# Kernel tuning notes

Measured on AMD Instinct MI355X. Metric: run time of the kernel, lower is better.

## Reference

```python
import jax, jax.numpy as jnp
import numpy as np

N_NODES = 100000
N_EDGES = 1600000
NEG_SLOPE = 0.2
EPS = 1e-16


def gat_conv(x, edge_index, W, att_src, att_dst, bias, heads, out_ch, concat):
    # x: [N, F_in]; edge_index: [2, E] with edge (src j -> dst i)
    N = x.shape[0]
    src, dst = edge_index[0], edge_index[1]
    h = (x @ W).reshape(N, heads, out_ch)              # [N, H, C]
    a_src = (h * att_src[None]).sum(-1)                # [N, H]
    a_dst = (h * att_dst[None]).sum(-1)                # [N, H]
    e = a_src[src] + a_dst[dst]                        # [E, H]
    e = jnp.where(e > 0, e, NEG_SLOPE * e)             # LeakyReLU(0.2)
    # segment softmax over destination node
    m = jax.ops.segment_max(e, dst, num_segments=N)    # [N, H]
    m = jnp.where(jnp.isfinite(m), m, 0.0)
    ex = jnp.exp(e - m[dst])                           # [E, H]
    s = jax.ops.segment_sum(ex, dst, num_segments=N)   # [N, H]
    alpha = ex / (s[dst] + EPS)                        # [E, H]
    msg = h[src] * alpha[..., None]                    # [E, H, C]
    out = jax.ops.segment_sum(msg, dst, num_segments=N)  # [N, H, C]
    if concat:
        out = out.reshape(N, heads * out_ch)
    else:
        out = out.mean(axis=1)
    return out + bias


def setup_inputs() -> dict:
    key = jax.random.key(0)
    ks = jax.random.split(key, 8)
    x = jax.random.normal(ks[0], (N_NODES, 2), dtype=jnp.float32)
    edge_index = jax.random.randint(ks[1], (2, N_EDGES), 0, N_NODES, dtype=jnp.int64)
    glorot = lambda k, shape, fan: jax.random.normal(k, shape, jnp.float32) * (1.0 / np.sqrt(fan))
    W1 = glorot(ks[2], (2, 128), 2)
    att_src1 = glorot(ks[3], (8, 16), 16)
    att_dst1 = glorot(ks[4], (8, 16), 16)
    b1 = jnp.zeros((128,), jnp.float32)
    W2 = glorot(ks[5], (128, 4), 128)
    att_src2 = glorot(ks[6], (1, 4), 4)
    att_dst2 = glorot(ks[7], (1, 4), 4)
    b2 = jnp.zeros((4,), jnp.float32)
    return {"x": x, "edge_index": edge_index, "W1": W1, "att_src1": att_src1,
            "att_dst1": att_dst1, "b1": b1, "W2": W2, "att_src2": att_src2,
            "att_dst2": att_dst2, "b2": b2}


def reference(x, edge_index, W1, att_src1, att_dst1, b1, W2, att_src2, att_dst2, b2):
    h = gat_conv(x, edge_index, W1, att_src1, att_dst1, b1, heads=8, out_ch=16, concat=True)
    h = jax.nn.relu(h)
    # dropout p=0.6 is identity in eval mode
    h = gat_conv(h, edge_index, W2, att_src2, att_dst2, b2, heads=1, out_ch=4, concat=True)
    return jax.nn.log_softmax(h, axis=1)
```

## Files before the change

### kernel.cpp

```cpp
#include <hip/hip_runtime.h>
#include <math.h>

static constexpr float kNegSlope = 0.2f;
static constexpr float kEps = 1e-16f;
static constexpr int SLICES = 256;
static constexpr int BSHIFT = 7;
static constexpr int BMASK = 127;
static constexpr unsigned SRCMASK = 0x1FFFFu;
static constexpr int CAP = 2816;

__device__ __forceinline__ float leaky(float v) {
    return v > 0.0f ? v : kNegSlope * v;
}


__global__ __launch_bounds__(512) void k_hist1(const int* __restrict__ ei,
                                               int* __restrict__ table,
                                               int* __restrict__ rowptr,
                                               int E, int N, int NBUCK) {
    __shared__ int hist[832];
    int b = blockIdx.x, t = threadIdx.x;
    if (b == 0 && t == 0) rowptr[N] = E;
    for (int i = t; i < NBUCK; i += 512) hist[i] = 0;
    __syncthreads();
    int S = (((E + SLICES - 1) / SLICES) + 3) & ~3;
    int lo = b * S, hi = min(lo + S, E);
    for (int i = lo + t * 4; i < hi; i += 512 * 4) {
        int4 dv = *(const int4*)(ei + E + i);
        atomicAdd(&hist[dv.x >> BSHIFT], 1);
        atomicAdd(&hist[dv.y >> BSHIFT], 1);
        atomicAdd(&hist[dv.z >> BSHIFT], 1);
        atomicAdd(&hist[dv.w >> BSHIFT], 1);
    }
    __syncthreads();
    for (int i = t; i < NBUCK; i += 512) table[i * SLICES + b] = hist[i];
}

__global__ __launch_bounds__(256) void k_scan_reduce(const int* __restrict__ src,
                                                     int* __restrict__ partial, int n) {
    __shared__ int wsum[4];
    int b = blockIdx.x, t = threadIdx.x;
    int base = b * 1024 + t * 4;
    int s = 0;
#pragma unroll
    for (int k = 0; k < 4; ++k) {
        int idx = base + k;
        s += (idx < n) ? src[idx] : 0;
    }
#pragma unroll
    for (int off = 1; off < 64; off <<= 1) s += __shfl_xor(s, off);
    if ((t & 63) == 0) wsum[t >> 6] = s;
    __syncthreads();
    if (t == 0) partial[b] = wsum[0] + wsum[1] + wsum[2] + wsum[3];
}

__global__ __launch_bounds__(256) void k_scan_apply(int* __restrict__ data,
                                                    const int* __restrict__ partial,
                                                    int n, int nsb) {
    __shared__ int sm[8];
    __shared__ int baseSh;
    int b = blockIdx.x, t = threadIdx.x;
    int acc = 0;
    for (int i = t; i < b; i += 256) acc += partial[i];
#pragma unroll
    for (int off = 1; off < 64; off <<= 1) acc += __shfl_xor(acc, off);
    if ((t & 63) == 0) sm[t >> 6] = acc;
    __syncthreads();
    if (t == 0) baseSh = sm[0] + sm[1] + sm[2] + sm[3];
    __syncthreads();
    int chunkBase = baseSh;
    __syncthreads();
    int base = b * 1024 + t * 4;
    int v[4];
#pragma unroll
    for (int k = 0; k < 4; ++k) {
        int idx = base + k;
        v[k] = (idx < n) ? data[idx] : 0;
    }
    int sum4 = v[0] + v[1] + v[2] + v[3];
    int s = sum4;
#pragma unroll
    for (int off = 1; off < 64; off <<= 1) {
        int u = __shfl_up(s, off);
        if ((t & 63) >= off) s += u;
    }
    if ((t & 63) == 63) sm[t >> 6] = s;
    __syncthreads();
    int woff = 0;
    int w = t >> 6;
    for (int ww = 0; ww < w; ++ww) woff += sm[ww];
    int ex = chunkBase + woff + (s - sum4);
#pragma unroll
    for (int k = 0; k < 4; ++k) {
        int idx = base + k;
        if (idx < n) data[idx] = ex;
        ex += v[k];
    }
}

__global__ __launch_bounds__(512) void k_bin2(const int* __restrict__ ei,
                                              const int* __restrict__ table,
                                              unsigned* __restrict__ sbuf, int E, int NBUCK) {
    __shared__ int cur[832];
    int b = blockIdx.x, t = threadIdx.x;
    for (int i = t; i < NBUCK; i += 512) cur[i] = table[i * SLICES + b];
    __syncthreads();
    int S = (((E + SLICES - 1) / SLICES) + 3) & ~3;
    int lo = b * S, hi = min(lo + S, E);
    for (int i = lo + t * 4; i < hi; i += 512 * 4) {
        int4 sv = *(const int4*)(ei + i);
        int4 dv = *(const int4*)(ei + E + i);
        int pos;
        pos = atomicAdd(&cur[dv.x >> BSHIFT], 1);
        sbuf[pos] = (unsigned)sv.x | ((unsigned)(dv.x & BMASK) << 17);
        pos = atomicAdd(&cur[dv.y >> BSHIFT], 1);
        sbuf[pos] = (unsigned)sv.y | ((unsigned)(dv.y & BMASK) << 17);
        pos = atomicAdd(&cur[dv.z >> BSHIFT], 1);
        sbuf[pos] = (unsigned)sv.z | ((unsigned)(dv.z & BMASK) << 17);
        pos = atomicAdd(&cur[dv.w >> BSHIFT], 1);
        sbuf[pos] = (unsigned)sv.w | ((unsigned)(dv.w & BMASK) << 17);
    }
}

__global__ __launch_bounds__(512) void k_sort(
        const unsigned* __restrict__ sbuf, const int* __restrict__ table,
        int* __restrict__ rowptr, int* __restrict__ ssrc,
        int N, int E, int NBUCK) {
    __shared__ int hist[128];
    __shared__ int sc[128];
    __shared__ int cur[128];
    __shared__ unsigned raws[CAP];
    __shared__ int sls[CAP];
    int b = blockIdx.x;
    int t = threadIdx.x;
    int lo = table[b * SLICES];
    int hi = (b + 1 < NBUCK) ? table[(b + 1) * SLICES] : E;
    int cnt = hi - lo;
    bool inLds = (cnt <= CAP);

    if (t < 128) hist[t] = 0;
    __syncthreads();

    if (inLds) {
        for (int i = t; i < cnt; i += 512) {
            unsigned v = sbuf[lo + i];
            raws[i] = v;
            atomicAdd(&hist[v >> 17], 1);
        }
    } else {
        for (int i = lo + t; i < hi; i += 512) atomicAdd(&hist[sbuf[i] >> 17], 1);
    }
    __syncthreads();

    if (t < 128) {
        int lane = t & 63;
        int own = hist[t];
        int v = own;
#pragma unroll
        for (int off = 1; off < 64; off <<= 1) {
            int u = __shfl_up(v, off);
            if (lane >= off) v += u;
        }
        sc[t] = v;
    }
    __syncthreads();
    if (t < 128) {
        int ex = sc[t] - hist[t] + (t >= 64 ? sc[63] : 0);
        cur[t] = ex;
        int node = (b << BSHIFT) + t;
        if (node < N) rowptr[node] = lo + ex;
    }
    __syncthreads();

    if (inLds) {
        for (int i = t; i < cnt; i += 512) {
            unsigned v = raws[i];
            int pos = atomicAdd(&cur[v >> 17], 1);
            sls[pos] = (int)(v & SRCMASK);
        }
        __syncthreads();
        for (int i = t; i < cnt; i += 512) ssrc[lo + i] = sls[i];
    } else {
        for (int i = lo + t; i < hi; i += 512) {
            unsigned v = sbuf[i];
            int pos = atomicAdd(&cur[v >> 17], 1);
            ssrc[lo + pos] = (int)(v & SRCMASK);
        }
    }
}

__global__ __launch_bounds__(256) void k_fill(const int* __restrict__ ssrc,
                                              const float* __restrict__ x,
                                              float* __restrict__ sxy, int E) {
    int i4 = (blockIdx.x * 256 + threadIdx.x) * 4;
    const float2* x2 = (const float2*)x;
    if (i4 + 3 < E) {
        int4 s = *(const int4*)(ssrc + i4);
        float2 a = x2[s.x];
        float2 b = x2[s.y];
        float2 c = x2[s.z];
        float2 d = x2[s.w];
        *(float4*)(sxy + 2 * i4)     = make_float4(a.x, a.y, b.x, b.y);
        *(float4*)(sxy + 2 * i4 + 4) = make_float4(c.x, c.y, d.x, d.y);
    } else {
        for (int i = i4; i < E; ++i) {
            float2 a = x2[ssrc[i]];
            sxy[2 * i] = a.x;
            sxy[2 * i + 1] = a.y;
        }
    }
}

__global__ __launch_bounds__(256) void k_gather1(
        const int* __restrict__ rowptr, const float* __restrict__ sxy,
        const float* __restrict__ x,
        const float* __restrict__ W1, const float* __restrict__ att_src1,
        const float* __restrict__ att_dst1, const float* __restrict__ b1,
        const float* __restrict__ W2, float* __restrict__ h2, int N) {
    __shared__ float pbuf[32];
    int t = threadIdx.x;
    if (t < 32) {
        int which = t >> 4;
        int hd = t & 15;
        int h = hd >> 1, d = hd & 1;
        const float* att = which ? att_dst1 : att_src1;
        float s = 0.0f;
#pragma unroll
        for (int c = 0; c < 16; ++c) s += W1[d * 128 + h * 16 + c] * att[h * 16 + c];
        pbuf[which * 16 + d * 8 + h] = s;
    }
    __syncthreads();

    int idx = blockIdx.x * blockDim.x + t;
    int n = idx >> 3, q = idx & 7;
    if (n >= N) return;
    const float2* x2 = (const float2*)x;
    const float2* sx2 = (const float2*)sxy;
    int start = rowptr[n], end = rowptr[n + 1];
    float2 xn = x2[n];
    float Ps0[8], Ps1[8], adv[8], l[8], s0[8], s1[8];
#pragma unroll
    for (int h = 0; h < 8; ++h) {
        Ps0[h] = pbuf[h];
        Ps1[h] = pbuf[8 + h];
        adv[h] = xn.x * pbuf[16 + h] + xn.y * pbuf[24 + h];
        l[h] = 0.f; s0[h] = 0.f; s1[h] = 0.f;
    }
    for (int j = start + q; j < end; j += 8) {
        float2 xs = sx2[j];
#pragma unroll
        for (int h = 0; h < 8; ++h) {
            float p = __expf(leaky(xs.x * Ps0[h] + xs.y * Ps1[h] + adv[h]));
            l[h] += p; s0[h] += p * xs.x; s1[h] += p * xs.y;
        }
    }
#pragma unroll
    for (int off = 1; off < 8; off <<= 1) {
#pragma unroll
        for (int h = 0; h < 8; ++h) {
            l[h] += __shfl_xor(l[h], off);
            s0[h] += __shfl_xor(s0[h], off);
            s1[h] += __shfl_xor(s1[h], off);
        }
    }
    float h0 = 0.f, h1v = 0.f, h2v = 0.f, h3 = 0.f;
    {
        float inv = 1.0f / (l[q] + kEps);
        float sX0 = s0[q] * inv, sX1 = s1[q] * inv;
#pragma unroll
        for (int c = 0; c < 16; ++c) {
            int col = q * 16 + c;
            float o = fmaxf(W1[col] * sX0 + W1[128 + col] * sX1 + b1[col], 0.0f);
            h0 += o * W2[col * 4 + 0];
            h1v += o * W2[col * 4 + 1];
            h2v += o * W2[col * 4 + 2];
            h3 += o * W2[col * 4 + 3];
        }
    }
#pragma unroll
    for (int off = 1; off < 8; off <<= 1) {
        h0 += __shfl_xor(h0, off);
        h1v += __shfl_xor(h1v, off);
        h2v += __shfl_xor(h2v, off);
        h3 += __shfl_xor(h3, off);
    }
    if (q == 0) {
        ((float4*)h2)[n] = make_float4(h0, h1v, h2v, h3);
    }
}

__global__ __launch_bounds__(256) void k_gather2_out(
        const int* __restrict__ rowptr, const int* __restrict__ ssrc,
        const float* __restrict__ h2, const float* __restrict__ att_src2,
        const float* __restrict__ att_dst2, const float* __restrict__ b2,
        float* __restrict__ out, int N) {
    int idx = blockIdx.x * blockDim.x + threadIdx.x;
    int n = idx >> 3, q = idx & 7;
    if (n >= N) return;
    int start = rowptr[n], end = rowptr[n + 1];
    float4 as2 = *(const float4*)att_src2;
    float4 ad2v = *(const float4*)att_dst2;
    const float4* h4 = (const float4*)h2;
    float4 hn = h4[n];
    float ad = hn.x * ad2v.x + hn.y * ad2v.y + hn.z * ad2v.z + hn.w * ad2v.w;
    float l = 0.0f;
    float4 acc = make_float4(0.f, 0.f, 0.f, 0.f);
    int j = start + q;
    for (; j + 8 < end; j += 16) {
        int s0 = ssrc[j];
        int s1 = ssrc[j + 8];
        float4 ha = h4[s0];
        float4 hb = h4[s1];
        float e0 = ha.x * as2.x + ha.y * as2.y + ha.z * as2.z + ha.w * as2.w + ad;
        float e1 = hb.x * as2.x + hb.y * as2.y + hb.z * as2.z + hb.w * as2.w + ad;
        float p0 = __expf(leaky(e0));
        float p1 = __expf(leaky(e1));
        l += p0 + p1;
        acc.x += p0 * ha.x + p1 * hb.x;
        acc.y += p0 * ha.y + p1 * hb.y;
        acc.z += p0 * ha.z + p1 * hb.z;
        acc.w += p0 * ha.w + p1 * hb.w;
    }
    if (j < end) {
        int s0 = ssrc[j];
        float4 ha = h4[s0];
        float e0 = ha.x * as2.x + ha.y * as2.y + ha.z * as2.z + ha.w * as2.w + ad;
        float p0 = __expf(leaky(e0));
        l += p0;
        acc.x += p0 * ha.x;
        acc.y += p0 * ha.y;
        acc.z += p0 * ha.z;
        acc.w += p0 * ha.w;
    }
#pragma unroll
    for (int off = 1; off < 8; off <<= 1) {
        l += __shfl_xor(l, off);
        acc.x += __shfl_xor(acc.x, off);
        acc.y += __shfl_xor(acc.y, off);
        acc.z += __shfl_xor(acc.z, off);
        acc.w += __shfl_xor(acc.w, off);
    }
    if (q == 0) {
        float inv = 1.0f / (l + kEps);
        float4 v = make_float4(acc.x * inv + b2[0], acc.y * inv + b2[1],
                               acc.z * inv + b2[2], acc.w * inv + b2[3]);
        float mx = fmaxf(fmaxf(v.x, v.y), fmaxf(v.z, v.w));
        float sum = __expf(v.x - mx) + __expf(v.y - mx) + __expf(v.z - mx) + __expf(v.w - mx);
        float lse = mx + logf(sum);
        ((float4*)out)[n] = make_float4(v.x - lse, v.y - lse, v.z - lse, v.w - lse);
    }
}

extern "C" void kernel_launch(void* const* d_in, const int* in_sizes, int n_in,
                              void* d_out, int out_size, void* d_ws, size_t ws_size,
                              hipStream_t stream) {
    const float* x        = (const float*)d_in[0];
    const int*   ei       = (const int*)d_in[1];
    const float* W1       = (const float*)d_in[2];
    const float* att_src1 = (const float*)d_in[3];
    const float* att_dst1 = (const float*)d_in[4];
    const float* b1       = (const float*)d_in[5];
    const float* W2       = (const float*)d_in[6];
    const float* att_src2 = (const float*)d_in[7];
    const float* att_dst2 = (const float*)d_in[8];
    const float* b2       = (const float*)d_in[9];

    const int N = in_sizes[0] / 2;
    const int E = in_sizes[1] / 2;
    const int NBUCK = (N + BMASK) >> BSHIFT;
    const int ntable = NBUCK * SLICES;
    const int nsb = (ntable + 1023) / 1024;
    const int Epad = (E + 3) & ~3;

    int* table     = (int*)d_ws;
    int* partial   = table + ntable + 64;
    int* rowptr    = partial + 1024;
    int* ssrc      = rowptr + ((N + 4) & ~3);
    unsigned* sbuf = (unsigned*)(ssrc + Epad);
    float* sxy     = (float*)sbuf;
    float* h2      = (float*)((int*)sbuf + 2 * (size_t)Epad);

    k_hist1<<<SLICES, 512, 0, stream>>>(ei, table, rowptr, E, N, NBUCK);
    k_scan_reduce<<<nsb, 256, 0, stream>>>(table, partial, ntable);
    k_scan_apply<<<nsb, 256, 0, stream>>>(table, partial, ntable, nsb);
    k_bin2<<<SLICES, 512, 0, stream>>>(ei, table, sbuf, E, NBUCK);

    k_sort<<<NBUCK, 512, 0, stream>>>(sbuf, table, rowptr, ssrc, N, E, NBUCK);

    k_fill<<<((E + 3) / 4 + 255) / 256, 256, 0, stream>>>(ssrc, x, sxy, E);

    k_gather1<<<(N * 8 + 255) / 256, 256, 0, stream>>>(rowptr, sxy, x,
                                                       W1, att_src1, att_dst1, b1,
                                                       W2, h2, N);

    k_gather2_out<<<(N * 8 + 255) / 256, 256, 0, stream>>>(rowptr, ssrc, h2,
                                                           att_src2, att_dst2, b2,
                                                           (float*)d_out, N);
}
```

Baseline: 172.7 us.

## Drop k_fill gather pass, gather x directly in gather1, split fold into own kernel

Removes the k_fill kernel that materialised sorted x pairs per edge, and has k_gather1 read x through ssrc indices directly, with a 2-way unrolled edge loop to overlap the indirect loads. The per-node projection through W1, ReLU and W2 moves from the tail of k_gather1 into a new k_fold kernel that uses one thread per node with weights staged in LDS. This avoids writing and rereading a 12.8 MB edge-sized buffer. In exchange it adds random 8-byte gathers of x (800 KB, likely cache-resident), a new 6.4 MB intermediate for attA/attB, and an extra kernel launch.

```diff
diff --git a/kernel.cpp b/kernel.cpp
--- a/kernel.cpp
+++ b/kernel.cpp
@@ -189,34 +189,12 @@
     }
 }
 
-__global__ __launch_bounds__(256) void k_fill(const int* __restrict__ ssrc,
-                                              const float* __restrict__ x,
-                                              float* __restrict__ sxy, int E) {
-    int i4 = (blockIdx.x * 256 + threadIdx.x) * 4;
-    const float2* x2 = (const float2*)x;
-    if (i4 + 3 < E) {
-        int4 s = *(const int4*)(ssrc + i4);
-        float2 a = x2[s.x];
-        float2 b = x2[s.y];
-        float2 c = x2[s.z];
-        float2 d = x2[s.w];
-        *(float4*)(sxy + 2 * i4)     = make_float4(a.x, a.y, b.x, b.y);
-        *(float4*)(sxy + 2 * i4 + 4) = make_float4(c.x, c.y, d.x, d.y);
-    } else {
-        for (int i = i4; i < E; ++i) {
-            float2 a = x2[ssrc[i]];
-            sxy[2 * i] = a.x;
-            sxy[2 * i + 1] = a.y;
-        }
-    }
-}
-
 __global__ __launch_bounds__(256) void k_gather1(
-        const int* __restrict__ rowptr, const float* __restrict__ sxy,
+        const int* __restrict__ rowptr, const int* __restrict__ ssrc,
         const float* __restrict__ x,
         const float* __restrict__ W1, const float* __restrict__ att_src1,
-        const float* __restrict__ att_dst1, const float* __restrict__ b1,
-        const float* __restrict__ W2, float* __restrict__ h2, int N) {
+        const float* __restrict__ att_dst1,
+        float* __restrict__ attA, float* __restrict__ attB, int N) {
     __shared__ float pbuf[32];
     int t = threadIdx.x;
     if (t < 32) {
@@ -235,7 +213,6 @@
     int n = idx >> 3, q = idx & 7;
     if (n >= N) return;
     const float2* x2 = (const float2*)x;
-    const float2* sx2 = (const float2*)sxy;
     int start = rowptr[n], end = rowptr[n + 1];
     float2 xn = x2[n];
     float Ps0[8], Ps1[8], adv[8], l[8], s0[8], s1[8];
@@ -246,12 +223,30 @@
         adv[h] = xn.x * pbuf[16 + h] + xn.y * pbuf[24 + h];
         l[h] = 0.f; s0[h] = 0.f; s1[h] = 0.f;
     }
-    for (int j = start + q; j < end; j += 8) {
-        float2 xs = sx2[j];
+    int j = start + q;
+    for (; j + 8 < end; j += 16) {
+        int sa = ssrc[j];
+        int sb = ssrc[j + 8];
+        float2 xa = x2[sa];
+        float2 xb = x2[sb];
 #pragma unroll
         for (int h = 0; h < 8; ++h) {
-            float p = __expf(leaky(xs.x * Ps0[h] + xs.y * Ps1[h] + adv[h]));
-            l[h] += p; s0[h] += p * xs.x; s1[h] += p * xs.y;
+            float pa = __expf(leaky(xa.x * Ps0[h] + xa.y * Ps1[h] + adv[h]));
+            float pb = __expf(leaky(xb.x * Ps0[h] + xb.y * Ps1[h] + adv[h]));
+            l[h] += pa + pb;
+            s0[h] += pa * xa.x + pb * xb.x;
+            s1[h] += pa * xa.y + pb * xb.y;
+        }
+    }
+    if (j < end) {
+        int sa = ssrc[j];
+        float2 xa = x2[sa];
+#pragma unroll
+        for (int h = 0; h < 8; ++h) {
+            float pa = __expf(leaky(xa.x * Ps0[h] + xa.y * Ps1[h] + adv[h]));
+            l[h] += pa;
+            s0[h] += pa * xa.x;
+            s1[h] += pa * xa.y;
         }
     }
 #pragma unroll
@@ -263,30 +258,51 @@
             s1[h] += __shfl_xor(s1[h], off);
         }
     }
-    float h0 = 0.f, h1v = 0.f, h2v = 0.f, h3 = 0.f;
-    {
-        float inv = 1.0f / (l[q] + kEps);
-        float sX0 = s0[q] * inv, sX1 = s1[q] * inv;
+    float inv = 1.0f / (l[q] + kEps);
+    attA[n * 8 + q] = s0[q] * inv;
+    attB[n * 8 + q] = s1[q] * inv;
+}
+
+__global__ __launch_bounds__(256) void k_fold(
+        const float* __restrict__ attA, const float* __restrict__ attB,
+        const float* __restrict__ W1, const float* __restrict__ b1,
+        const float* __restrict__ W2, float* __restrict__ h2, int N) {
+    __shared__ float4 pk1[128];
+    __shared__ float4 pk2[128];
+    int t = threadIdx.x;
+    if (t < 128) {
+        pk1[t] = make_float4(W1[t], W1[128 + t], b1[t], 0.f);
+        pk2[t] = ((const float4*)W2)[t];
+    }
+    __syncthreads();
+    int n = blockIdx.x * 256 + t;
+    if (n >= N) return;
+    const float4* A = (const float4*)(attA + n * 8);
+    const float4* B = (const float4*)(attB + n * 8);
+    float4 a01 = A[0], a23 = A[1];
+    float4 b01 = B[0], b23 = B[1];
+    float4 acc = make_float4(0.f, 0.f, 0.f, 0.f);
+#pragma unroll
+    for (int h = 0; h < 8; ++h) {
+        float sx0 = (h == 0) ? a01.x : (h == 1) ? a01.y : (h == 2) ? a01.z :
+                    (h == 3) ? a01.w : (h == 4) ? a23.x : (h == 5) ? a23.y :
+                    (h == 6) ? a23.z : a23.w;
+        float sx1 = (h == 0) ? b01.x : (h == 1) ? b01.y : (h == 2) ? b01.z :
+                    (h == 3) ? b01.w : (h == 4) ? b23.x : (h == 5) ? b23.y :
+                    (h == 6) ? b23.z : b23.w;
 #pragma unroll
         for (int c = 0; c < 16; ++c) {
-            int col = q * 16 + c;
-            float o = fmaxf(W1[col] * sX0 + W1[128 + col] * sX1 + b1[col], 0.0f);
-            h0 += o * W2[col * 4 + 0];
-            h1v += o * W2[col * 4 + 1];
-            h2v += o * W2[col * 4 + 2];
-            h3 += o * W2[col * 4 + 3];
-        }
-    }
-#pragma unroll
-    for (int off = 1; off < 8; off <<= 1) {
-        h0 += __shfl_xor(h0, off);
-        h1v += __shfl_xor(h1v, off);
-        h2v += __shfl_xor(h2v, off);
-        h3 += __shfl_xor(h3, off);
-    }
-    if (q == 0) {
-        ((float4*)h2)[n] = make_float4(h0, h1v, h2v, h3);
-    }
+            int col = h * 16 + c;
+            float4 p = pk1[col];
+            float o = fmaxf(p.x * sx0 + p.y * sx1 + p.z, 0.0f);
+            float4 w = pk2[col];
+            acc.x += o * w.x;
+            acc.y += o * w.y;
+            acc.z += o * w.z;
+            acc.w += o * w.w;
+        }
+    }
+    ((float4*)h2)[n] = acc;
 }
 
 __global__ __launch_bounds__(256) void k_gather2_out(
@@ -370,15 +386,16 @@
     const int NBUCK = (N + BMASK) >> BSHIFT;
     const int ntable = NBUCK * SLICES;
     const int nsb = (ntable + 1023) / 1024;
-    const int Epad = (E + 3) & ~3;
 
     int* table     = (int*)d_ws;
     int* partial   = table + ntable + 64;
     int* rowptr    = partial + 1024;
     int* ssrc      = rowptr + ((N + 4) & ~3);
-    unsigned* sbuf = (unsigned*)(ssrc + Epad);
-    float* sxy     = (float*)sbuf;
-    float* h2      = (float*)((int*)sbuf + 2 * (size_t)Epad);
+    unsigned* sbuf = (unsigned*)(ssrc + E);
+    float* attA    = (float*)sbuf;
+    float* attB    = attA + (size_t)N * 8;
+    size_t post    = (size_t)E > (size_t)N * 16 ? (size_t)E : (size_t)N * 16;
+    float* h2      = (float*)(sbuf + post);
 
     k_hist1<<<SLICES, 512, 0, stream>>>(ei, table, rowptr, E, N, NBUCK);
     k_scan_reduce<<<nsb, 256, 0, stream>>>(table, partial, ntable);
@@ -387,11 +404,10 @@
 
     k_sort<<<NBUCK, 512, 0, stream>>>(sbuf, table, rowptr, ssrc, N, E, NBUCK);
 
-    k_fill<<<((E + 3) / 4 + 255) / 256, 256, 0, stream>>>(ssrc, x, sxy, E);
-
-    k_gather1<<<(N * 8 + 255) / 256, 256, 0, stream>>>(rowptr, sxy, x,
-                                                       W1, att_src1, att_dst1, b1,
-                                                       W2, h2, N);
+    k_gather1<<<(N * 8 + 255) / 256, 256, 0, stream>>>(rowptr, ssrc, x,
+                                                       W1, att_src1, att_dst1,
+                                                       attA, attB, N);
+    k_fold<<<(N + 255) / 256, 256, 0, stream>>>(attA, attB, W1, b1, W2, h2, N);
 
     k_gather2_out<<<(N * 8 + 255) / 256, 256, 0, stream>>>(rowptr, ssrc, h2,
                                                            att_src2, att_dst2, b2,
```

Result: faster. 151.2 us (-12.4%).
